# Optimization experiments

Measured on AMD Instinct MI355X. Metric: run time of the kernel, lower is better.

The kernel has to match this reference:

```python
import jax, jax.numpy as jnp
import numpy as np
import math

ALPHA = 0.5
GAMMA_ALPHA = math.gamma(ALPHA)

def _xavier(key, fan_in, fan_out):
    limit = math.sqrt(6.0 / (fan_in + fan_out))
    return jax.random.uniform(key, (fan_in, fan_out), jnp.float32, -limit, limit)

def setup_inputs() -> dict:
    key = jax.random.key(0)
    ks = jax.random.split(key, 8)
    B, T, D_IN, H, D_OUT = 512, 1024, 64, 256, 64
    x = jax.random.normal(ks[0], (B, D_IN), jnp.float32)
    t = jnp.arange(T, dtype=jnp.float32) * 0.01  # increasing time grid
    W0 = _xavier(ks[1], D_IN + 1, H); b0 = jnp.zeros((H,), jnp.float32)
    W1 = _xavier(ks[2], H, H);        b1 = jnp.zeros((H,), jnp.float32)
    W2 = _xavier(ks[3], H, H);        b2 = jnp.zeros((H,), jnp.float32)
    W3 = _xavier(ks[4], H, D_OUT);    b3 = jnp.zeros((D_OUT,), jnp.float32)
    return {"x": x, "t": t, "W0": W0, "b0": b0, "W1": W1, "b1": b1,
            "W2": W2, "b2": b2, "W3": W3, "b3": b3}

def reference(x, t, W0, b0, W1, b1, W2, b2, W3, b3):
    # Fractional Euler: y_i = y_{i-1} + (dt^alpha / Gamma(alpha)) * tanh(MLP([t_{i-1}, y_{i-1}]))
    B = x.shape[0]
    y0 = x  # input_dim == output_dim, so initial state is x directly
    t_prev = t[:-1]            # [T-1]
    dt = t[1:] - t[:-1]        # [T-1]

    def mlp(tp, state):
        h = jnp.concatenate([jnp.full((B, 1), tp, dtype=state.dtype), state], axis=-1)
        h = h @ W0 + b0
        h = h @ W1 + b1  # nn.Sequential has no activations between linears
        h = h @ W2 + b2
        h = h @ W3 + b3
        return jnp.tanh(h)  # single tanh applied in ode_func

    def step(state, inputs):
        tp, d = inputs
        deriv = mlp(tp, state)
        factor = (d ** ALPHA) / GAMMA_ALPHA
        new = state + factor * deriv
        return new, new

    _, traj = jax.lax.scan(step, y0, (t_prev, dt))   # traj: [T-1, B, D_OUT]
    solution = jnp.concatenate([y0[:, None, :], jnp.swapaxes(traj, 0, 1)], axis=1)
    return solution  # [B, T, D_OUT]
```

## Files before the change

### kernel.cpp

```cpp
#include <hip/hip_runtime.h>
#include <math.h>

#define HDIM 256
#define DDIM 64
#define BROWS 512
#define TSTEPS 1024
#define AROWS 66

typedef float f32x2 __attribute__((ext_vector_type(2)));
typedef float f32x4 __attribute__((ext_vector_type(4)));

__global__ void compose1(const float* __restrict__ W0, const float* __restrict__ b0,
                         const float* __restrict__ W1, const float* __restrict__ b1,
                         float* __restrict__ out1) {
    int r = blockIdx.x;
    int c = threadIdx.x;
    const float* arow = (r < 65) ? (W0 + r * HDIM) : b0;
    float acc = (r == 65) ? b1[c] : 0.0f;
    for (int h = 0; h < HDIM; ++h)
        acc = fmaf(arow[h], W1[h * HDIM + c], acc);
    out1[r * HDIM + c] = acc;
}

__global__ void compose2(const float* __restrict__ in1,
                         const float* __restrict__ W2, const float* __restrict__ b2,
                         float* __restrict__ out2) {
    int r = blockIdx.x, c = threadIdx.x;
    const float* arow = in1 + r * HDIM;
    float acc = (r == 65) ? b2[c] : 0.0f;
    for (int h = 0; h < HDIM; ++h)
        acc = fmaf(arow[h], W2[h * HDIM + c], acc);
    out2[r * HDIM + c] = acc;
}

__global__ void compose3(const float* __restrict__ in2,
                         const float* __restrict__ W3, const float* __restrict__ b3,
                         float* __restrict__ out3) {
    int r = blockIdx.x, c = threadIdx.x;
    const float* arow = in2 + r * HDIM;
    float acc = (r == 65) ? b3[c] : 0.0f;
    for (int h = 0; h < HDIM; ++h)
        acc = fmaf(arow[h], W3[h * DDIM + c], acc);
    out3[r * DDIM + c] = acc;
}

__device__ __forceinline__ void pkfma(f32x2& acc, f32x2 a, f32x2 b) {
    asm("v_pk_fma_f32 %0, %1, %2, %0" : "+v"(acc) : "v"(a), "v"(b));
}

__launch_bounds__(64, 1)
__global__ void fode_scan(const float* __restrict__ x, const float* __restrict__ t,
                          const float* __restrict__ Weff,
                          float* __restrict__ out) {
    const int b = blockIdx.x;
    const int d = threadIdx.x;

    __shared__ __align__(16) float ylds[DDIM];
    __shared__ __align__(8) float2 plds[TSTEPS];

    const float invG = 0.56418958354775628695f;
    const float K2L = 2.88539008177792681472f;

    for (int i = d; i < TSTEPS - 1; i += DDIM) {
        float t0 = t[i];
        float t1 = t[i + 1];
        float dt = t1 - t0;
        plds[i] = make_float2(dt, sqrtf(dt) * invG);
    }

    const int lo = d & 31;
    const int hh = d >> 5;

    f32x2 Wa[16], Wb[16];
#pragma unroll
    for (int c = 0; c < 16; ++c) {
        int j = 32 * hh + 2 * c;
        Wa[c].x = K2L * Weff[(1 + j) * DDIM + lo];
        Wa[c].y = K2L * Weff[(2 + j) * DDIM + lo];
        Wb[c].x = K2L * Weff[(1 + j) * DDIM + lo + 32];
        Wb[c].y = K2L * Weff[(2 + j) * DDIM + lo + 32];
    }
    const float wts   = K2L * Weff[d];
    const float biass = K2L * Weff[65 * DDIM + d];

    auto cal = __builtin_amdgcn_permlane32_swap(d, d, false, false);
    const bool pick0 = (cal[0] == (d ^ 32));

    const unsigned ybase = (unsigned)(uintptr_t)&ylds[0];
    const unsigned waddr = ybase + 4u * (unsigned)d;
    const unsigned rbase = ybase + 128u * (unsigned)hh;
    const unsigned pbase = (unsigned)(uintptr_t)&plds[0];

    const float t0g = t[0];

    float y = x[b * DDIM + d];
    float* op = out + (size_t)b * TSTEPS * DDIM + d;
    *op = y;

#define READS8(r0,r1,r2,r3,r4,r5,r6,r7)                                   \
    asm volatile(                                                         \
        "ds_read_b128 %[o0], %[a] offset:0\n\t"                           \
        "ds_read_b128 %[o1], %[a] offset:16\n\t"                          \
        "ds_read_b128 %[o2], %[a] offset:32\n\t"                          \
        "ds_read_b128 %[o3], %[a] offset:48\n\t"                          \
        "ds_read_b128 %[o4], %[a] offset:64\n\t"                          \
        "ds_read_b128 %[o5], %[a] offset:80\n\t"                          \
        "ds_read_b128 %[o6], %[a] offset:96\n\t"                          \
        "ds_read_b128 %[o7], %[a] offset:112"                             \
        : [o0] "=&v"(r0), [o1] "=&v"(r1), [o2] "=&v"(r2), [o3] "=&v"(r3), \
          [o4] "=&v"(r4), [o5] "=&v"(r5), [o6] "=&v"(r6), [o7] "=&v"(r7)  \
        : [a] "v"(rbase))

#define QUADH(vq, c)                                                      \
    {                                                                     \
        f32x2 qlo = __builtin_shufflevector(vq, vq, 0, 1);                \
        f32x2 qhi = __builtin_shufflevector(vq, vq, 2, 3);                \
        pkfma(accA0, qlo, Wa[2 * (c) + 0]);                               \
        pkfma(accA1, qhi, Wa[2 * (c) + 1]);                               \
        pkfma(accB0, qlo, Wb[2 * (c) + 0]);                               \
        pkfma(accB1, qhi, Wb[2 * (c) + 1]);                               \
    }

    float s;
    {
        asm volatile("ds_write_b32 %0, %1" :: "v"(waddr), "v"(y));
        f32x4 v0, v1, v2, v3, v4, v5, v6, v7;
        READS8(v0, v1, v2, v3, v4, v5, v6, v7);
        float base0 = fmaf(t0g, wts, biass);
        asm volatile("s_waitcnt lgkmcnt(0)" ::: "memory");
        __builtin_amdgcn_sched_barrier(0);
        f32x2 accA0 = {0.f, 0.f}, accA1 = {0.f, 0.f};
        f32x2 accB0 = {0.f, 0.f}, accB1 = {0.f, 0.f};
        QUADH(v0, 0) QUADH(v1, 1) QUADH(v2, 2) QUADH(v3, 3)
        QUADH(v4, 4) QUADH(v5, 5) QUADH(v6, 6) QUADH(v7, 7)
        f32x2 ra = accA0 + accA1;  float qa = ra.x + ra.y;
        f32x2 rb = accB0 + accB1;  float qb = rb.x + rb.y;
        float keep = (d < 32) ? qa : qb;
        float send = (d < 32) ? qb : qa;
        auto sw = __builtin_amdgcn_permlane32_swap(__float_as_int(send),
                                                   __float_as_int(send), false, false);
        float recv = __int_as_float(pick0 ? sw[0] : sw[1]);
        s = base0 + (keep + recv);
    }

    f32x2 prm;
    prm.x = plds[0].x;
    prm.y = plds[0].y;

    for (int k = 0; k < TSTEPS - 1; ++k) {
        float e  = __builtin_amdgcn_exp2f(s);
        float th = fmaf(-2.0f, __builtin_amdgcn_rcpf(e + 1.0f), 1.0f);
        asm volatile("ds_write_b32 %0, %1" :: "v"(waddr), "v"(th));

        f32x4 v0, v1, v2, v3, v4, v5, v6, v7;
        READS8(v0, v1, v2, v3, v4, v5, v6, v7);
        f32x2 prmn;
        unsigned paddr = pbase + 8u * (unsigned)(k + 1);
        asm volatile("ds_read_b64 %0, %1" : "=&v"(prmn) : "v"(paddr));

        y = fmaf(prm.y, th, y);
        op += DDIM;
        *op = y;
        float sc = fmaf(prm.x, wts, s);

        f32x2 accA0 = {0.f, 0.f}, accA1 = {0.f, 0.f};
        f32x2 accB0 = {0.f, 0.f}, accB1 = {0.f, 0.f};

        asm volatile("s_waitcnt lgkmcnt(5)" ::: "memory");
        __builtin_amdgcn_sched_barrier(0);
        QUADH(v0, 0) QUADH(v1, 1) QUADH(v2, 2) QUADH(v3, 3)

        asm volatile("s_waitcnt lgkmcnt(1)" ::: "memory");
        __builtin_amdgcn_sched_barrier(0);
        QUADH(v4, 4) QUADH(v5, 5) QUADH(v6, 6) QUADH(v7, 7)

        f32x2 ra = accA0 + accA1;  float qa = ra.x + ra.y;
        f32x2 rb = accB0 + accB1;  float qb = rb.x + rb.y;
        float keep = (d < 32) ? qa : qb;
        float send = (d < 32) ? qb : qa;
        auto sw = __builtin_amdgcn_permlane32_swap(__float_as_int(send),
                                                   __float_as_int(send), false, false);
        float recv = __int_as_float(pick0 ? sw[0] : sw[1]);
        float dotT = keep + recv;

        s = fmaf(prm.y, dotT, sc);

        asm volatile("s_waitcnt lgkmcnt(0)" ::: "memory");
        __builtin_amdgcn_sched_barrier(0);
        prm = prmn;
    }
#undef QUADH
#undef READS8
}

extern "C" void kernel_launch(void* const* d_in, const int* in_sizes, int n_in,
                              void* d_out, int out_size, void* d_ws, size_t ws_size,
                              hipStream_t stream) {
    const float* x  = (const float*)d_in[0];
    const float* t  = (const float*)d_in[1];
    const float* W0 = (const float*)d_in[2];
    const float* b0 = (const float*)d_in[3];
    const float* W1 = (const float*)d_in[4];
    const float* b1 = (const float*)d_in[5];
    const float* W2 = (const float*)d_in[6];
    const float* b2 = (const float*)d_in[7];
    const float* W3 = (const float*)d_in[8];
    const float* b3 = (const float*)d_in[9];
    float* out = (float*)d_out;

    float* buf1 = (float*)d_ws;
    float* buf2 = buf1 + AROWS * HDIM;
    float* buf3 = buf2 + AROWS * HDIM;

    compose1<<<AROWS, HDIM, 0, stream>>>(W0, b0, W1, b1, buf1);
    compose2<<<AROWS, HDIM, 0, stream>>>(buf1, W2, b2, buf2);
    compose3<<<AROWS, DDIM, 0, stream>>>(buf2, W3, b3, buf3);
    fode_scan<<<BROWS, DDIM, 0, stream>>>(x, t, buf3, out);
}
```

Baseline: 237.5 us.

## Interleave two batch rows per wavefront and fold tanh affine into weights

Each 64-thread block now runs two independent batch rows, interleaving their LDS write/read, dot product and transcendental chains. The latency of one row's serial chain can then hide behind the other's. tanh is rewritten as 1-2r with r=1/(exp+1): the -2 goes into the weights and the constant becomes a precomputed row-sum term Cd, shortening the per-step dependency chain. The cost is half as many blocks (256 wavefronts on the GPU), more registers, and small floating-point reassociation differences.

```diff
diff --git a/kernel.cpp b/kernel.cpp
--- a/kernel.cpp
+++ b/kernel.cpp
@@ -52,11 +52,12 @@
 __global__ void fode_scan(const float* __restrict__ x, const float* __restrict__ t,
                           const float* __restrict__ Weff,
                           float* __restrict__ out) {
-    const int b = blockIdx.x;
-    const int d = threadIdx.x;
-
-    __shared__ __align__(16) float ylds[DDIM];
-    __shared__ __align__(8) float2 plds[TSTEPS];
+    const int bA = blockIdx.x * 2;
+    const int d  = threadIdx.x;
+
+    __shared__ __align__(16) float yAl[DDIM];
+    __shared__ __align__(16) float yBl[DDIM];
+    __shared__ __align__(8)  float2 plds[TSTEPS];
 
     const float invG = 0.56418958354775628695f;
     const float K2L = 2.88539008177792681472f;
@@ -75,29 +76,37 @@
 #pragma unroll
     for (int c = 0; c < 16; ++c) {
         int j = 32 * hh + 2 * c;
-        Wa[c].x = K2L * Weff[(1 + j) * DDIM + lo];
-        Wa[c].y = K2L * Weff[(2 + j) * DDIM + lo];
-        Wb[c].x = K2L * Weff[(1 + j) * DDIM + lo + 32];
-        Wb[c].y = K2L * Weff[(2 + j) * DDIM + lo + 32];
+        Wa[c].x = -2.0f * K2L * Weff[(1 + j) * DDIM + lo];
+        Wa[c].y = -2.0f * K2L * Weff[(2 + j) * DDIM + lo];
+        Wb[c].x = -2.0f * K2L * Weff[(1 + j) * DDIM + lo + 32];
+        Wb[c].y = -2.0f * K2L * Weff[(2 + j) * DDIM + lo + 32];
     }
     const float wts   = K2L * Weff[d];
     const float biass = K2L * Weff[65 * DDIM + d];
+    float Cd = 0.0f;
+    for (int j = 0; j < DDIM; ++j) Cd += Weff[(1 + j) * DDIM + d];
+    Cd *= K2L;
 
     auto cal = __builtin_amdgcn_permlane32_swap(d, d, false, false);
     const bool pick0 = (cal[0] == (d ^ 32));
 
-    const unsigned ybase = (unsigned)(uintptr_t)&ylds[0];
-    const unsigned waddr = ybase + 4u * (unsigned)d;
-    const unsigned rbase = ybase + 128u * (unsigned)hh;
-    const unsigned pbase = (unsigned)(uintptr_t)&plds[0];
-
+    const unsigned yAbase = (unsigned)(uintptr_t)&yAl[0];
+    const unsigned yBbase = (unsigned)(uintptr_t)&yBl[0];
+    const unsigned waddrA = yAbase + 4u * (unsigned)d;
+    const unsigned waddrB = yBbase + 4u * (unsigned)d;
+    const unsigned rbaseA = yAbase + 128u * (unsigned)hh;
+    const unsigned rbaseB = yBbase + 128u * (unsigned)hh;
+    const unsigned pbase  = (unsigned)(uintptr_t)&plds[0];
     const float t0g = t[0];
 
-    float y = x[b * DDIM + d];
-    float* op = out + (size_t)b * TSTEPS * DDIM + d;
-    *op = y;
-
-#define READS8(r0,r1,r2,r3,r4,r5,r6,r7)                                   \
+    float yA = x[bA * DDIM + d];
+    float yB = x[(bA + 1) * DDIM + d];
+    float* opA = out + (size_t)bA * TSTEPS * DDIM + d;
+    float* opB = opA + (size_t)TSTEPS * DDIM;
+    *opA = yA;
+    *opB = yB;
+
+#define READS8(r0,r1,r2,r3,r4,r5,r6,r7, BASE)                             \
     asm volatile(                                                         \
         "ds_read_b128 %[o0], %[a] offset:0\n\t"                           \
         "ds_read_b128 %[o1], %[a] offset:16\n\t"                          \
@@ -109,38 +118,53 @@
         "ds_read_b128 %[o7], %[a] offset:112"                             \
         : [o0] "=&v"(r0), [o1] "=&v"(r1), [o2] "=&v"(r2), [o3] "=&v"(r3), \
           [o4] "=&v"(r4), [o5] "=&v"(r5), [o6] "=&v"(r6), [o7] "=&v"(r7)  \
-        : [a] "v"(rbase))
-
-#define QUADH(vq, c)                                                      \
+        : [a] "v"(BASE))
+
+#define DOT_TAIL(v0,v1,v2,v3,v4,v5,v6,v7, DOTOUT)                         \
     {                                                                     \
-        f32x2 qlo = __builtin_shufflevector(vq, vq, 0, 1);                \
-        f32x2 qhi = __builtin_shufflevector(vq, vq, 2, 3);                \
-        pkfma(accA0, qlo, Wa[2 * (c) + 0]);                               \
-        pkfma(accA1, qhi, Wa[2 * (c) + 1]);                               \
-        pkfma(accB0, qlo, Wb[2 * (c) + 0]);                               \
-        pkfma(accB1, qhi, Wb[2 * (c) + 1]);                               \
-    }
-
-    float s;
+        f32x2 accA0 = {0.f, 0.f}, accA1 = {0.f, 0.f};                     \
+        f32x2 accB0 = {0.f, 0.f}, accB1 = {0.f, 0.f};                     \
+        f32x4 vv_[8] = {v0, v1, v2, v3, v4, v5, v6, v7};                  \
+        _Pragma("unroll")                                                 \
+        for (int c = 0; c < 8; ++c) {                                     \
+            f32x2 qlo = __builtin_shufflevector(vv_[c], vv_[c], 0, 1);    \
+            f32x2 qhi = __builtin_shufflevector(vv_[c], vv_[c], 2, 3);    \
+            pkfma(accA0, qlo, Wa[2 * c + 0]);                             \
+            pkfma(accA1, qhi, Wa[2 * c + 1]);                             \
+            pkfma(accB0, qlo, Wb[2 * c + 0]);                             \
+            pkfma(accB1, qhi, Wb[2 * c + 1]);                             \
+        }                                                                 \
+        f32x2 ra = accA0 + accA1;                                         \
+        f32x2 rb = accB0 + accB1;                                         \
+        float qa = ra.x + ra.y;                                           \
+        float qb = rb.x + rb.y;                                           \
+        float keep = (d < 32) ? qa : qb;                                  \
+        float send = (d < 32) ? qb : qa;                                  \
+        auto sw2 = __builtin_amdgcn_permlane32_swap(__float_as_int(send), \
+                                         __float_as_int(send), false, false);\
+        float recv = __int_as_float(pick0 ? sw2[0] : sw2[1]);             \
+        DOTOUT = keep + recv;                                             \
+    }
+
+    float sA, sB, rA, rB;
     {
-        asm volatile("ds_write_b32 %0, %1" :: "v"(waddr), "v"(y));
-        f32x4 v0, v1, v2, v3, v4, v5, v6, v7;
-        READS8(v0, v1, v2, v3, v4, v5, v6, v7);
+        asm volatile("s_waitcnt lgkmcnt(0)" ::: "memory");
+        asm volatile("ds_write_b32 %0, %1" :: "v"(waddrA), "v"(yA));
+        asm volatile("ds_write_b32 %0, %1" :: "v"(waddrB), "v"(yB));
+        f32x4 a0, a1, a2, a3, a4, a5, a6, a7;
+        f32x4 b0, b1, b2, b3, b4, b5, b6, b7;
+        READS8(a0, a1, a2, a3, a4, a5, a6, a7, rbaseA);
+        READS8(b0, b1, b2, b3, b4, b5, b6, b7, rbaseB);
         float base0 = fmaf(t0g, wts, biass);
         asm volatile("s_waitcnt lgkmcnt(0)" ::: "memory");
         __builtin_amdgcn_sched_barrier(0);
-        f32x2 accA0 = {0.f, 0.f}, accA1 = {0.f, 0.f};
-        f32x2 accB0 = {0.f, 0.f}, accB1 = {0.f, 0.f};
-        QUADH(v0, 0) QUADH(v1, 1) QUADH(v2, 2) QUADH(v3, 3)
-        QUADH(v4, 4) QUADH(v5, 5) QUADH(v6, 6) QUADH(v7, 7)
-        f32x2 ra = accA0 + accA1;  float qa = ra.x + ra.y;
-        f32x2 rb = accB0 + accB1;  float qb = rb.x + rb.y;
-        float keep = (d < 32) ? qa : qb;
-        float send = (d < 32) ? qb : qa;
-        auto sw = __builtin_amdgcn_permlane32_swap(__float_as_int(send),
-                                                   __float_as_int(send), false, false);
-        float recv = __int_as_float(pick0 ? sw[0] : sw[1]);
-        s = base0 + (keep + recv);
+        float dotYA, dotYB;
+        DOT_TAIL(a0, a1, a2, a3, a4, a5, a6, a7, dotYA);
+        DOT_TAIL(b0, b1, b2, b3, b4, b5, b6, b7, dotYB);
+        sA = fmaf(-0.5f, dotYA, base0);
+        sB = fmaf(-0.5f, dotYB, base0);
+        rA = __builtin_amdgcn_rcpf(__builtin_amdgcn_exp2f(sA) + 1.0f);
+        rB = __builtin_amdgcn_rcpf(__builtin_amdgcn_exp2f(sB) + 1.0f);
     }
 
     f32x2 prm;
@@ -148,48 +172,44 @@
     prm.y = plds[0].y;
 
     for (int k = 0; k < TSTEPS - 1; ++k) {
-        float e  = __builtin_amdgcn_exp2f(s);
-        float th = fmaf(-2.0f, __builtin_amdgcn_rcpf(e + 1.0f), 1.0f);
-        asm volatile("ds_write_b32 %0, %1" :: "v"(waddr), "v"(th));
-
-        f32x4 v0, v1, v2, v3, v4, v5, v6, v7;
-        READS8(v0, v1, v2, v3, v4, v5, v6, v7);
+        asm volatile("ds_write_b32 %0, %1" :: "v"(waddrA), "v"(rA));
+        f32x4 a0, a1, a2, a3, a4, a5, a6, a7;
+        READS8(a0, a1, a2, a3, a4, a5, a6, a7, rbaseA);
+        asm volatile("ds_write_b32 %0, %1" :: "v"(waddrB), "v"(rB));
+        f32x4 b0, b1, b2, b3, b4, b5, b6, b7;
+        READS8(b0, b1, b2, b3, b4, b5, b6, b7, rbaseB);
         f32x2 prmn;
         unsigned paddr = pbase + 8u * (unsigned)(k + 1);
         asm volatile("ds_read_b64 %0, %1" : "=&v"(prmn) : "v"(paddr));
 
-        y = fmaf(prm.y, th, y);
-        op += DDIM;
-        *op = y;
-        float sc = fmaf(prm.x, wts, s);
-
-        f32x2 accA0 = {0.f, 0.f}, accA1 = {0.f, 0.f};
-        f32x2 accB0 = {0.f, 0.f}, accB1 = {0.f, 0.f};
-
-        asm volatile("s_waitcnt lgkmcnt(5)" ::: "memory");
-        __builtin_amdgcn_sched_barrier(0);
-        QUADH(v0, 0) QUADH(v1, 1) QUADH(v2, 2) QUADH(v3, 3)
+        float dt = prm.x, f = prm.y;
+        float scA = fmaf(f, Cd, fmaf(dt, wts, sA));
+        float scB = fmaf(f, Cd, fmaf(dt, wts, sB));
+        float m2f = -2.0f * f;
+        yA = fmaf(m2f, rA, yA + f);
+        yB = fmaf(m2f, rB, yB + f);
+        opA += DDIM; *opA = yA;
+        opB += DDIM; *opB = yB;
+
+        asm volatile("s_waitcnt lgkmcnt(10)" ::: "memory");
+        __builtin_amdgcn_sched_barrier(0);
+        float dotA;
+        DOT_TAIL(a0, a1, a2, a3, a4, a5, a6, a7, dotA);
+        sA = fmaf(f, dotA, scA);
+        rA = __builtin_amdgcn_rcpf(__builtin_amdgcn_exp2f(sA) + 1.0f);
 
         asm volatile("s_waitcnt lgkmcnt(1)" ::: "memory");
         __builtin_amdgcn_sched_barrier(0);
-        QUADH(v4, 4) QUADH(v5, 5) QUADH(v6, 6) QUADH(v7, 7)
-
-        f32x2 ra = accA0 + accA1;  float qa = ra.x + ra.y;
-        f32x2 rb = accB0 + accB1;  float qb = rb.x + rb.y;
-        float keep = (d < 32) ? qa : qb;
-        float send = (d < 32) ? qb : qa;
-        auto sw = __builtin_amdgcn_permlane32_swap(__float_as_int(send),
-                                                   __float_as_int(send), false, false);
-        float recv = __int_as_float(pick0 ? sw[0] : sw[1]);
-        float dotT = keep + recv;
-
-        s = fmaf(prm.y, dotT, sc);
+        float dotB;
+        DOT_TAIL(b0, b1, b2, b3, b4, b5, b6, b7, dotB);
+        sB = fmaf(f, dotB, scB);
+        rB = __builtin_amdgcn_rcpf(__builtin_amdgcn_exp2f(sB) + 1.0f);
 
         asm volatile("s_waitcnt lgkmcnt(0)" ::: "memory");
         __builtin_amdgcn_sched_barrier(0);
         prm = prmn;
     }
-#undef QUADH
+#undef DOT_TAIL
 #undef READS8
 }
 
@@ -215,5 +235,5 @@
     compose1<<<AROWS, HDIM, 0, stream>>>(W0, b0, W1, b1, buf1);
     compose2<<<AROWS, HDIM, 0, stream>>>(buf1, W2, b2, buf2);
     compose3<<<AROWS, DDIM, 0, stream>>>(buf2, W3, b3, buf3);
-    fode_scan<<<BROWS, DDIM, 0, stream>>>(x, t, buf3, out);
-}
+    fode_scan<<<BROWS / 2, DDIM, 0, stream>>>(x, t, buf3, out);
+}
```

Result: slower. 355.2 us (+49.5%).

## Rewrite tanh recurrence via reciprocal form and pack two steps' params per LDS read

Applied to the files above, without the earlier changes.

Rewrites tanh(z) = 1 - 2r with r = 1/(exp(2z)+1), so each step writes r to LDS instead of tanh. The -2 factor is folded into the weights and a per-column constant Cd (the weight column sum) is added, which takes the fma that built th off the serial chain. The time-step parameters are packed two per float4, and the loop is unrolled by two so one ds_read_b128 serves two steps, with the waitcnt counts adjusted to match. This shortens the per-step critical path at the cost of slightly different rounding and an extra epilogue step.

```diff
diff --git a/kernel.cpp b/kernel.cpp
--- a/kernel.cpp
+++ b/kernel.cpp
@@ -56,16 +56,23 @@
     const int d = threadIdx.x;
 
     __shared__ __align__(16) float ylds[DDIM];
-    __shared__ __align__(8) float2 plds[TSTEPS];
+    __shared__ __align__(16) float4 plds4[TSTEPS / 2];
 
     const float invG = 0.56418958354775628695f;
     const float K2L = 2.88539008177792681472f;
 
-    for (int i = d; i < TSTEPS - 1; i += DDIM) {
-        float t0 = t[i];
-        float t1 = t[i + 1];
-        float dt = t1 - t0;
-        plds[i] = make_float2(dt, sqrtf(dt) * invG);
+    for (int i = d; i < TSTEPS / 2; i += DDIM) {
+        int k0 = 2 * i, k1 = 2 * i + 1;
+        float ta = t[k0], tb = t[k0 + 1];
+        float dt0 = tb - ta;
+        float f0 = sqrtf(dt0) * invG;
+        float dt1 = 0.f, f1 = 0.f;
+        if (k1 + 1 < TSTEPS) {
+            float tc = t[k1 + 1];
+            dt1 = tc - tb;
+            f1 = sqrtf(dt1) * invG;
+        }
+        plds4[i] = make_float4(dt0, f0, dt1, f1);
     }
 
     const int lo = d & 31;
@@ -75,13 +82,16 @@
 #pragma unroll
     for (int c = 0; c < 16; ++c) {
         int j = 32 * hh + 2 * c;
-        Wa[c].x = K2L * Weff[(1 + j) * DDIM + lo];
-        Wa[c].y = K2L * Weff[(2 + j) * DDIM + lo];
-        Wb[c].x = K2L * Weff[(1 + j) * DDIM + lo + 32];
-        Wb[c].y = K2L * Weff[(2 + j) * DDIM + lo + 32];
+        Wa[c].x = -2.0f * K2L * Weff[(1 + j) * DDIM + lo];
+        Wa[c].y = -2.0f * K2L * Weff[(2 + j) * DDIM + lo];
+        Wb[c].x = -2.0f * K2L * Weff[(1 + j) * DDIM + lo + 32];
+        Wb[c].y = -2.0f * K2L * Weff[(2 + j) * DDIM + lo + 32];
     }
     const float wts   = K2L * Weff[d];
     const float biass = K2L * Weff[65 * DDIM + d];
+    float Cd = 0.0f;
+    for (int j = 0; j < DDIM; ++j) Cd += Weff[(1 + j) * DDIM + d];
+    Cd *= K2L;
 
     auto cal = __builtin_amdgcn_permlane32_swap(d, d, false, false);
     const bool pick0 = (cal[0] == (d ^ 32));
@@ -89,8 +99,7 @@
     const unsigned ybase = (unsigned)(uintptr_t)&ylds[0];
     const unsigned waddr = ybase + 4u * (unsigned)d;
     const unsigned rbase = ybase + 128u * (unsigned)hh;
-    const unsigned pbase = (unsigned)(uintptr_t)&plds[0];
-
+    const unsigned pbase = (unsigned)(uintptr_t)&plds4[0];
     const float t0g = t[0];
 
     float y = x[b * DDIM + d];
@@ -121,8 +130,9 @@
         pkfma(accB1, qhi, Wb[2 * (c) + 1]);                               \
     }
 
-    float s;
+    float s, r;
     {
+        asm volatile("s_waitcnt lgkmcnt(0)" ::: "memory");
         asm volatile("ds_write_b32 %0, %1" :: "v"(waddr), "v"(y));
         f32x4 v0, v1, v2, v3, v4, v5, v6, v7;
         READS8(v0, v1, v2, v3, v4, v5, v6, v7);
@@ -133,62 +143,70 @@
         f32x2 accB0 = {0.f, 0.f}, accB1 = {0.f, 0.f};
         QUADH(v0, 0) QUADH(v1, 1) QUADH(v2, 2) QUADH(v3, 3)
         QUADH(v4, 4) QUADH(v5, 5) QUADH(v6, 6) QUADH(v7, 7)
-        f32x2 ra = accA0 + accA1;  float qa = ra.x + ra.y;
-        f32x2 rb = accB0 + accB1;  float qb = rb.x + rb.y;
+        f32x2 ra = accA0 + accA1, rb = accB0 + accB1;
+        float qa = ra.x + ra.y, qb = rb.x + rb.y;
+        float send = (d < 32) ? qb : qa;
+        auto sw2 = __builtin_amdgcn_permlane32_swap(__float_as_int(send),
+                                                    __float_as_int(send), false, false);
         float keep = (d < 32) ? qa : qb;
-        float send = (d < 32) ? qb : qa;
-        auto sw = __builtin_amdgcn_permlane32_swap(__float_as_int(send),
-                                                   __float_as_int(send), false, false);
-        float recv = __int_as_float(pick0 ? sw[0] : sw[1]);
-        s = base0 + (keep + recv);
-    }
-
-    f32x2 prm;
-    prm.x = plds[0].x;
-    prm.y = plds[0].y;
-
-    for (int k = 0; k < TSTEPS - 1; ++k) {
-        float e  = __builtin_amdgcn_exp2f(s);
-        float th = fmaf(-2.0f, __builtin_amdgcn_rcpf(e + 1.0f), 1.0f);
-        asm volatile("ds_write_b32 %0, %1" :: "v"(waddr), "v"(th));
-
-        f32x4 v0, v1, v2, v3, v4, v5, v6, v7;
-        READS8(v0, v1, v2, v3, v4, v5, v6, v7);
-        f32x2 prmn;
-        unsigned paddr = pbase + 8u * (unsigned)(k + 1);
-        asm volatile("ds_read_b64 %0, %1" : "=&v"(prmn) : "v"(paddr));
-
-        y = fmaf(prm.y, th, y);
+        float base2 = fmaf(-0.5f, keep, base0);
+        float recv = __int_as_float(pick0 ? sw2[0] : sw2[1]);
+        s = fmaf(-0.5f, recv, base2);
+        r = __builtin_amdgcn_rcpf(__builtin_amdgcn_exp2f(s) + 1.0f);
+    }
+
+    f32x4 prm4 = *(const f32x4*)&plds4[0];
+
+#define STEP_BODY(DT, F, PREFETCH_STMT, W1CNT, W2CNT)                     \
+    {                                                                     \
+        asm volatile("ds_write_b32 %0, %1" :: "v"(waddr), "v"(r));        \
+        f32x4 v0, v1, v2, v3, v4, v5, v6, v7;                             \
+        READS8(v0, v1, v2, v3, v4, v5, v6, v7);                           \
+        PREFETCH_STMT;                                                    \
+        float dt = (DT), f = (F);                                         \
+        float sc = fmaf(f, Cd, fmaf(dt, wts, s));                         \
+        y = fmaf(-2.0f * f, r, y + f);                                    \
+        op += DDIM;                                                       \
+        *op = y;                                                          \
+        f32x2 accA0 = {0.f, 0.f}, accA1 = {0.f, 0.f};                     \
+        f32x2 accB0 = {0.f, 0.f}, accB1 = {0.f, 0.f};                     \
+        asm volatile("s_waitcnt lgkmcnt(" #W1CNT ")" ::: "memory");       \
+        __builtin_amdgcn_sched_barrier(0);                                \
+        QUADH(v0, 0) QUADH(v1, 1) QUADH(v2, 2) QUADH(v3, 3)               \
+        asm volatile("s_waitcnt lgkmcnt(" #W2CNT ")" ::: "memory");       \
+        __builtin_amdgcn_sched_barrier(0);                                \
+        QUADH(v4, 4) QUADH(v5, 5) QUADH(v6, 6) QUADH(v7, 7)               \
+        f32x2 ra = accA0 + accA1, rb = accB0 + accB1;                     \
+        float qa = ra.x + ra.y, qb = rb.x + rb.y;                         \
+        float send = (d < 32) ? qb : qa;                                  \
+        auto sw2 = __builtin_amdgcn_permlane32_swap(__float_as_int(send), \
+                                         __float_as_int(send), false, false);\
+        float keep = (d < 32) ? qa : qb;                                  \
+        float base2 = fmaf(f, keep, sc);                                  \
+        float recv = __int_as_float(pick0 ? sw2[0] : sw2[1]);             \
+        s = fmaf(f, recv, base2);                                         \
+        r = __builtin_amdgcn_rcpf(__builtin_amdgcn_exp2f(s) + 1.0f);      \
+    }
+
+    f32x4 prm4n;
+    for (int i = 0; i < TSTEPS / 2 - 1; ++i) {
+        STEP_BODY(prm4.x, prm4.y, , 4, 0)
+        unsigned paddr = pbase + 16u * (unsigned)(i + 1);
+        STEP_BODY(prm4.z, prm4.w,
+                  asm volatile("ds_read_b128 %0, %1" : "=&v"(prm4n) : "v"(paddr)),
+                  5, 1)
+        asm volatile("s_waitcnt lgkmcnt(0)" ::: "memory");
+        __builtin_amdgcn_sched_barrier(0);
+        prm4 = prm4n;
+    }
+
+    {
+        float f = prm4.y;
+        y = fmaf(-2.0f * f, r, y + f);
         op += DDIM;
         *op = y;
-        float sc = fmaf(prm.x, wts, s);
-
-        f32x2 accA0 = {0.f, 0.f}, accA1 = {0.f, 0.f};
-        f32x2 accB0 = {0.f, 0.f}, accB1 = {0.f, 0.f};
-
-        asm volatile("s_waitcnt lgkmcnt(5)" ::: "memory");
-        __builtin_amdgcn_sched_barrier(0);
-        QUADH(v0, 0) QUADH(v1, 1) QUADH(v2, 2) QUADH(v3, 3)
-
-        asm volatile("s_waitcnt lgkmcnt(1)" ::: "memory");
-        __builtin_amdgcn_sched_barrier(0);
-        QUADH(v4, 4) QUADH(v5, 5) QUADH(v6, 6) QUADH(v7, 7)
-
-        f32x2 ra = accA0 + accA1;  float qa = ra.x + ra.y;
-        f32x2 rb = accB0 + accB1;  float qb = rb.x + rb.y;
-        float keep = (d < 32) ? qa : qb;
-        float send = (d < 32) ? qb : qa;
-        auto sw = __builtin_amdgcn_permlane32_swap(__float_as_int(send),
-                                                   __float_as_int(send), false, false);
-        float recv = __int_as_float(pick0 ? sw[0] : sw[1]);
-        float dotT = keep + recv;
-
-        s = fmaf(prm.y, dotT, sc);
-
-        asm volatile("s_waitcnt lgkmcnt(0)" ::: "memory");
-        __builtin_amdgcn_sched_barrier(0);
-        prm = prmn;
-    }
+    }
+#undef STEP_BODY
 #undef QUADH
 #undef READS8
 }
```

After: 229.5 us. -3.4%, faster.
